# Performance work log

Measured on AMD Instinct MI355X. Metric: run time of the kernel, lower is better.

Reference implementation:

```python
import jax, jax.numpy as jnp
import numpy as np

N = 128          # cube side (voxels)
LPIX = 3.0       # Mpc per voxel (hardcoded in dsq_loss.forward)
KBINS = 100      # radial k bins (hardcoded)
LOSS_WEIGHT = 1.0


def _binning(n, lpix, kbins):
    # Static radial k-bin assignment computed once with numpy.
    kf = 2.0 * np.pi * np.fft.fftfreq(n, d=lpix)
    kx, ky, kz = np.meshgrid(kf, kf, kf, indexing='ij')
    kmag = np.sqrt(kx * kx + ky * ky + kz * kz).ravel()  # [n^3]
    pos = kmag > 0
    edges = np.linspace(kmag[pos].min(), kmag.max(), kbins + 1)
    ids = np.clip(np.digitize(kmag, edges) - 1, 0, kbins - 1)
    ids = np.where(pos, ids, kbins)  # route k=0 (DC) mode to a dropped bin
    counts = np.bincount(ids[pos], minlength=kbins).astype(np.float32)
    kcent = 0.5 * (edges[:-1] + edges[1:])
    return ids.astype(np.int32), counts, kcent.astype(np.float32)

_IDS, _COUNTS, _KCENT = _binning(N, LPIX, KBINS)


def _dsq(x):
    # x: [B, 1, N, N, N] -> dimensionless power spectrum Delta^2(k): [B, KBINS]
    b = x.shape[0]
    fk = jnp.fft.fftn(x, axes=(-3, -2, -1))
    # P(k) estimator: |delta_k|^2 * Lpix^3 / N^3  (Lpix^6/V with V=(N*Lpix)^3)
    pk = (fk.real ** 2 + fk.imag ** 2) * (LPIX ** 3 / float(N ** 3))
    pk = pk.reshape(b, -1).T  # [N^3, B]
    sums = jax.ops.segment_sum(pk, jnp.asarray(_IDS), num_segments=KBINS + 1)[:KBINS]
    cnt = jnp.asarray(_COUNTS)[:, None]
    pmean = jnp.where(cnt > 0, sums / jnp.maximum(cnt, 1.0), jnp.nan)  # [KBINS, B]
    kc = jnp.asarray(_KCENT)[:, None]
    dsq = pmean * kc ** 3 / (2.0 * jnp.pi ** 2)
    return dsq.T  # [B, KBINS]


def setup_inputs() -> dict:
    key = jax.random.key(0)
    k1, k2 = jax.random.split(key)
    # positive brightness-temperature-like fields so log10(Delta^2) is finite
    pred = jax.random.uniform(k1, (8, 1, N, N, N), dtype=jnp.float32) + 0.1
    target = jax.random.uniform(k2, (8, 1, N, N, N), dtype=jnp.float32) + 0.1
    return {"pred": pred, "target": target}


def reference(pred, target):
    dsq_hr = _dsq(target)
    dsq_sr = _dsq(pred)
    loss = jnp.nanmean(jnp.abs(jnp.log10(dsq_hr) - jnp.log10(dsq_sr)))
    return LOSS_WEIGHT * loss
```

## Files before the change

### kernel.cpp

```cpp
#include <hip/hip_runtime.h>
#include <math.h>

#ifndef M_PI
#define M_PI 3.14159265358979323846
#endif

#define NSIDE 128
#define NVOX  2097152
#define KBINS 100
#define NFIELDS 16
#define NORMF (27.0f / 2097152.0f)
#define FSTRIDE ((size_t)65 * 16384)

#define WS_SUMS_OFF   0
#define WS_CNT_OFF    6464
#define WS_OCT_OFF    8192
#define WS_TRANS_OFF  282880

__device__ __forceinline__ double bin_edge(int i, double start, double step, double stop) {
    if (i == 100) return stop;
    return __dadd_rn(__dmul_rn((double)i, step), start);
}

__device__ __forceinline__ void bin_params(double* start, double* step, double* stop) {
    const double inv   = 1.0 / 384.0;
    const double twopi = 2.0 * M_PI;
    double k1 = __dmul_rn(twopi, __dmul_rn(1.0, inv));
    *start = sqrt(__dadd_rn(__dadd_rn(0.0, 0.0), __dmul_rn(k1, k1)));
    double k64 = __dmul_rn(twopi, __dmul_rn(-64.0, inv));
    double s64 = __dmul_rn(k64, k64);
    *stop = sqrt(__dadd_rn(__dadd_rn(s64, s64), s64));
    *step = (*stop - *start) / 100.0;
}

__device__ int compute_bin(int ix, int iy, int iz) {
    const double inv   = 1.0 / 384.0;
    const double twopi = 2.0 * M_PI;
    double fx = (double)(ix < 64 ? ix : ix - 128);
    double fy = (double)(iy < 64 ? iy : iy - 128);
    double fz = (double)(iz < 64 ? iz : iz - 128);
    double kx = __dmul_rn(twopi, __dmul_rn(fx, inv));
    double ky = __dmul_rn(twopi, __dmul_rn(fy, inv));
    double kz = __dmul_rn(twopi, __dmul_rn(fz, inv));
    double sq = __dadd_rn(__dadd_rn(__dmul_rn(kx, kx), __dmul_rn(ky, ky)), __dmul_rn(kz, kz));
    double kmag = sqrt(sq);
    if (!(kmag > 0.0)) return 100;
    double start, step, stop;
    bin_params(&start, &step, &stop);
    double t = (kmag - start) / step;
    int c = (int)floor(t);
    if (c < -1) c = -1;
    if (c > 100) c = 100;
    while (c < 100 && kmag >= bin_edge(c + 1, start, step, stop)) ++c;
    while (c >= 0 && kmag < bin_edge(c, start, step, stop)) --c;
    if (c < 0) c = 0;
    if (c > 99) c = 99;
    return c;
}


__device__ __forceinline__ int br3(int v) { return ((v & 1) << 2) | (v & 2) | ((v >> 2) & 1); }
__device__ __forceinline__ int br4(int v) {
    return ((v & 1) << 3) | ((v & 2) << 1) | ((v & 4) >> 1) | ((v & 8) >> 3);
}

__device__ __forceinline__ float2 f2add(float2 a, float2 b) { return make_float2(a.x + b.x, a.y + b.y); }
__device__ __forceinline__ float2 f2sub(float2 a, float2 b) { return make_float2(a.x - b.x, a.y - b.y); }
__device__ __forceinline__ float2 cmul(float2 a, float2 w) {
    return make_float2(a.x * w.x - a.y * w.y, a.x * w.y + a.y * w.x);
}
__device__ __forceinline__ float2 twid(float r) {
    return make_float2(__builtin_amdgcn_cosf(r), __builtin_amdgcn_sinf(r));
}

__device__ __forceinline__ void fft128_r16(float2 r[16], int m) {
    const float fm = (float)m;
#pragma unroll
    for (int j = 0; j < 8; ++j) {
        float2 W = twid(-(fm + 8.0f * (float)j) * (1.0f / 128.0f));
        float2 a = r[j], b = r[j + 8];
        r[j]     = f2add(a, b);
        r[j + 8] = cmul(f2sub(a, b), W);
    }
#pragma unroll
    for (int j = 0; j < 4; ++j) {
        float2 W = twid(-(fm + 8.0f * (float)j) * (1.0f / 64.0f));
#pragma unroll
        for (int half = 0; half < 16; half += 8) {
            float2 a = r[half + j], b = r[half + j + 4];
            r[half + j]     = f2add(a, b);
            r[half + j + 4] = cmul(f2sub(a, b), W);
        }
    }
#pragma unroll
    for (int j = 0; j < 2; ++j) {
        float2 W = twid(-(fm + 8.0f * (float)j) * (1.0f / 32.0f));
#pragma unroll
        for (int q = 0; q < 16; q += 4) {
            float2 a = r[q + j], b = r[q + j + 2];
            r[q + j]     = f2add(a, b);
            r[q + j + 2] = cmul(f2sub(a, b), W);
        }
    }
    {
        float2 W = twid(-fm * (1.0f / 16.0f));
#pragma unroll
        for (int q = 0; q < 16; q += 2) {
            float2 a = r[q], b = r[q + 1];
            r[q]     = f2add(a, b);
            r[q + 1] = cmul(f2sub(a, b), W);
        }
    }
#pragma unroll
    for (int h = 4; h >= 2; h >>= 1) {
        bool hi = (m & h) != 0;
        float2 W = twid(-(float)(m & (h - 1)) / (float)(2 * h));
#pragma unroll
        for (int j = 0; j < 16; ++j) {
            float2 x = r[j];
            float2 v = make_float2(__shfl_xor(x.x, h, 64), __shfl_xor(x.y, h, 64));
            float2 s = f2add(x, v);
            float2 d = cmul(f2sub(v, x), W);
            r[j] = hi ? d : s;
        }
    }
    {
        bool hi = (m & 1) != 0;
#pragma unroll
        for (int j = 0; j < 16; ++j) {
            float2 x = r[j];
            float2 v = make_float2(__shfl_xor(x.x, 1, 64), __shfl_xor(x.y, 1, 64));
            r[j] = hi ? f2sub(v, x) : f2add(x, v);
        }
    }
}

__global__ __launch_bounds__(256) void k_zero(float* sums, int* counts) {
    int t = blockIdx.x * 256 + threadIdx.x;
    if (t < NFIELDS * 101) sums[t] = 0.0f;
    if (t < 101) counts[t] = 0;
}

__global__ __launch_bounds__(256) void k_oct(unsigned char* __restrict__ oct,
                                             int* __restrict__ counts) {
    __shared__ int lcnt[4][104];
    int tid = threadIdx.x;
#pragma unroll
    for (int j = tid; j < 4 * 104; j += 256) ((int*)lcnt)[j] = 0;
    __syncthreads();
    int idx = blockIdx.x * 256 + tid;
    if (idx < 65 * 65 * 65) {
        int c = idx % 65;
        int r = idx / 65;
        int b = r % 65;
        int a = r / 65;
        int id = compute_bin(a, b, c);
        oct[c * 4225 + a * 65 + b] = (unsigned char)id;
        if (id < 100) {
            int w = ((a == 0 || a == 64) ? 1 : 2) *
                    ((b == 0 || b == 64) ? 1 : 2) *
                    ((c == 0 || c == 64) ? 1 : 2);
            atomicAdd(&lcnt[tid & 3][id], w);
        }
    }
    __syncthreads();
    if (tid < 101) {
        int tot = lcnt[0][tid] + lcnt[1][tid] + lcnt[2][tid] + lcnt[3][tid];
        if (tot) atomicAdd(&counts[tid], tot);
    }
}

__global__ __launch_bounds__(256, 2) void k_fft_zy(const float* __restrict__ pred,
                                                   const float* __restrict__ target,
                                                   float2* __restrict__ A) {
    __shared__ float2 lds[65][130];
    int t = threadIdx.x;
    int m = t & 7, row = t >> 3;
    int x = blockIdx.x;
    int f = blockIdx.y;
    const float* in = (f < 8) ? (pred + (size_t)f * NVOX)
                              : (target + (size_t)(f - 8) * NVOX);

    int b3 = br3(m);
#pragma unroll
    for (int y0 = 0; y0 < 128; y0 += 32) {
        int y = y0 + row;
        const float* src = in + (size_t)x * 16384 + (size_t)y * 128;
        float2 r[16];
#pragma unroll
        for (int j = 0; j < 16; ++j) r[j] = make_float2(src[m + 8 * j], 0.0f);
        fft128_r16(r, m);
        if (b3 < 4) {
#pragma unroll
            for (int j = 0; j < 16; ++j) lds[16 * b3 + br4(j)][y] = r[j];
        } else if (b3 == 4) {
            lds[64][y] = r[0];
        }
    }
    __syncthreads();

    float2* basef = A + (size_t)f * FSTRIDE + (size_t)x * 128;
#pragma unroll
    for (int k0 = 0; k0 < 96; k0 += 32) {
        int kz = k0 + row;
        if (kz <= 64) {
            float2 r[16];
#pragma unroll
            for (int j = 0; j < 16; ++j) r[j] = lds[kz][m + 8 * j];
            fft128_r16(r, m);
            float2* dst = basef + (size_t)kz * 16384;
#pragma unroll
            for (int j = 0; j < 16; ++j) dst[m + 8 * j] = r[j];
        }
    }
}

__global__ __launch_bounds__(256, 6) void k_fft_x_bin(const float2* __restrict__ A,
                                                      const unsigned char* __restrict__ oct,
                                                      float* __restrict__ sums) {
    __shared__ float lbins[8][104];
    __shared__ unsigned char ltab[4225];
    int t = threadIdx.x;
    int m = t & 7, g = t >> 3;
    int kz = blockIdx.x >> 2;
    int s0 = (blockIdx.x & 3) << 5;
    int f = blockIdx.y;
    for (int j = t; j < 8 * 104; j += 256) ((float*)lbins)[j] = 0.0f;
    for (int j = t; j < 4225; j += 256) ltab[j] = oct[kz * 4225 + j];
    const float2* base = A + (size_t)f * FSTRIDE + (size_t)kz * 16384 + (s0 + g);
    float2 r[16];
#pragma unroll
    for (int j = 0; j < 16; ++j) r[j] = base[(size_t)(m + 8 * j) * 128];
    fft128_r16(r, m);
    __syncthreads();
    int p = s0 + g;
    int ky = (br3(p & 7) << 4) | br4(p >> 3);
    int mky = (ky <= 64) ? ky : 128 - ky;
    int b3x = br3(m) << 4;
#pragma unroll
    for (int j = 0; j < 16; ++j) {
        int kx = b3x | br4(j);
        int mkx = (kx <= 64) ? kx : 128 - kx;
        float pk = r[j].x * r[j].x + r[j].y * r[j].y;
        atomicAdd(&lbins[t & 7][ltab[mkx * 65 + mky]], pk);
    }
    __syncthreads();
    if (t < 101) {
        float wz = (kz == 0 || kz == 64) ? 1.0f : 2.0f;
        float v = lbins[0][t] + lbins[1][t] + lbins[2][t] + lbins[3][t] +
                  lbins[4][t] + lbins[5][t] + lbins[6][t] + lbins[7][t];
        if (v != 0.0f) atomicAdd(&sums[f * 101 + t], v * (NORMF) * wz);
    }
}

__global__ __launch_bounds__(128) void k_finalize(const float* __restrict__ sums,
                                                  const int* __restrict__ counts,
                                                  float* __restrict__ out) {
    __shared__ double ssum[128];
    __shared__ int scnt[128];
    int k = threadIdx.x;
    double local = 0.0;
    int nloc = 0;
    if (k < KBINS) {
        int c = counts[k];
        if (c > 0) {
            double start, step, stop;
            bin_params(&start, &step, &stop);
            double e0 = bin_edge(k, start, step, stop);
            double e1 = bin_edge(k + 1, start, step, stop);
            float kc  = (float)(0.5 * (e0 + e1));
            float kc3 = kc * kc * kc;
            const float two_pi2 = (float)(2.0 * M_PI * M_PI);
            float cf = (float)c;
            for (int b = 0; b < 8; ++b) {
                float pm_p = sums[b * 101 + k] / cf;
                float pm_t = sums[(8 + b) * 101 + k] / cf;
                float dsq_p = pm_p * kc3 / two_pi2;
                float dsq_t = pm_t * kc3 / two_pi2;
                float d = fabsf(log10f(dsq_t) - log10f(dsq_p));
                local += (double)d;
            }
            nloc = 8;
        }
    }
    ssum[k] = local;
    scnt[k] = nloc;
    __syncthreads();
    for (int off = 64; off > 0; off >>= 1) {
        if (k < off) { ssum[k] += ssum[k + off]; scnt[k] += scnt[k + off]; }
        __syncthreads();
    }
    if (k == 0) out[0] = (float)(ssum[0] / (double)scnt[0]);
}

extern "C" void kernel_launch(void* const* d_in, const int* in_sizes, int n_in,
                              void* d_out, int out_size, void* d_ws, size_t ws_size,
                              hipStream_t stream) {
    (void)in_sizes; (void)n_in; (void)out_size; (void)ws_size;
    const float* pred   = (const float*)d_in[0];
    const float* target = (const float*)d_in[1];
    float* out = (float*)d_out;
    char* ws = (char*)d_ws;

    float* sums        = (float*)(ws + WS_SUMS_OFF);
    int* counts        = (int*)(ws + WS_CNT_OFF);
    unsigned char* oct = (unsigned char*)(ws + WS_OCT_OFF);
    float2* A          = (float2*)(ws + WS_TRANS_OFF);

    k_zero<<<7, 256, 0, stream>>>(sums, counts);
    k_oct<<<(65 * 65 * 65 + 255) / 256, 256, 0, stream>>>(oct, counts);

    k_fft_zy<<<dim3(128, NFIELDS), 256, 0, stream>>>(pred, target, A);
    k_fft_x_bin<<<dim3(65 * 4, NFIELDS), 256, 0, stream>>>(A, oct, sums);

    k_finalize<<<1, 128, 0, stream>>>(sums, counts, out);
}
```

Before: 333.6 us.

## Vectorize z-FFT input loads with new contiguous FFT and retile intermediate layout

Replaces the strided per-element z-row loads with float4 loads of 16 contiguous samples per lane, paired with a new FFT variant (fft128_c16) that uses precomputed constant twiddles suited to that contiguous assignment. It changes the intermediate spectrum layout so both the y-pass stores and the x-pass loads touch more contiguous addresses, and pads the LDS row to 132. It also adds scheduling barriers after the loads. The new FFT and layout must stay consistent with the bit-reversal indexing used later, which adds correctness risk.

```diff
diff --git a/kernel.cpp b/kernel.cpp
--- a/kernel.cpp
+++ b/kernel.cpp
@@ -11,6 +11,7 @@
 #define NFIELDS 16
 #define NORMF (27.0f / 2097152.0f)
 #define FSTRIDE ((size_t)65 * 16384)
+
 
 #define WS_SUMS_OFF   0
 #define WS_CNT_OFF    6464
@@ -58,7 +59,6 @@
     return c;
 }
 
-
 __device__ __forceinline__ int br3(int v) { return ((v & 1) << 2) | (v & 2) | ((v >> 2) & 1); }
 __device__ __forceinline__ int br4(int v) {
     return ((v & 1) << 3) | ((v & 2) << 1) | ((v & 4) >> 1) | ((v & 8) >> 3);
@@ -131,6 +131,107 @@
             float2 x = r[j];
             float2 v = make_float2(__shfl_xor(x.x, 1, 64), __shfl_xor(x.y, 1, 64));
             r[j] = hi ? f2sub(v, x) : f2add(x, v);
+        }
+    }
+}
+
+__device__ __forceinline__ void fft128_c16(float2 r[16], int m) {
+    const float S2 = 0.70710678118654752f;
+    {
+        int q = m & 3;
+        float2 Wm = make_float2(q == 0 ? 1.f : (q == 1 ? S2 : (q == 2 ? 0.f : -S2)),
+                                q == 0 ? 0.f : (q == 2 ? -1.f : -S2));
+        bool hi = (m & 4) != 0;
+        const float2 C[16] = {
+            {1.f,0.f},{0.99879546f,-0.04906767f},{0.99518473f,-0.09801714f},
+            {0.98917651f,-0.14673047f},{0.98078528f,-0.19509032f},{0.97003125f,-0.24298018f},
+            {0.95694034f,-0.29028468f},{0.94154407f,-0.33688985f},{0.92387953f,-0.38268343f},
+            {0.90398929f,-0.42755509f},{0.88192126f,-0.47139674f},{0.85772861f,-0.51410274f},
+            {0.83146961f,-0.55557023f},{0.80320753f,-0.59569930f},{0.77301045f,-0.63439328f},
+            {0.74095113f,-0.67155895f} };
+#pragma unroll
+        for (int j = 0; j < 16; ++j) {
+            float2 x = r[j];
+            float2 v = make_float2(__shfl_xor(x.x, 4, 64), __shfl_xor(x.y, 4, 64));
+            float2 s = f2add(x, v);
+            float2 d = cmul(cmul(f2sub(v, x), Wm), C[j]);
+            r[j] = hi ? d : s;
+        }
+    }
+    {
+        bool w = (m & 1) != 0;
+        bool hi = (m & 2) != 0;
+        const float2 C[16] = {
+            {1.f,0.f},{0.99518473f,-0.09801714f},{0.98078528f,-0.19509032f},
+            {0.95694034f,-0.29028468f},{0.92387953f,-0.38268343f},{0.88192126f,-0.47139674f},
+            {0.83146961f,-0.55557023f},{0.77301045f,-0.63439328f},{S2,-S2},
+            {0.63439328f,-0.77301045f},{0.55557023f,-0.83146961f},{0.47139674f,-0.88192126f},
+            {0.38268343f,-0.92387953f},{0.29028468f,-0.95694034f},{0.19509032f,-0.98078528f},
+            {0.09801714f,-0.99518473f} };
+#pragma unroll
+        for (int j = 0; j < 16; ++j) {
+            float2 x = r[j];
+            float2 v = make_float2(__shfl_xor(x.x, 2, 64), __shfl_xor(x.y, 2, 64));
+            float2 s = f2add(x, v);
+            float2 d = f2sub(v, x);
+            d = w ? make_float2(d.y, -d.x) : d;
+            d = cmul(d, C[j]);
+            r[j] = hi ? d : s;
+        }
+    }
+    {
+        bool hi = (m & 1) != 0;
+        const float2 C[16] = {
+            {1.f,0.f},{0.98078528f,-0.19509032f},{0.92387953f,-0.38268343f},
+            {0.83146961f,-0.55557023f},{S2,-S2},{0.55557023f,-0.83146961f},
+            {0.38268343f,-0.92387953f},{0.19509032f,-0.98078528f},{0.f,-1.f},
+            {-0.19509032f,-0.98078528f},{-0.38268343f,-0.92387953f},{-0.55557023f,-0.83146961f},
+            {-S2,-S2},{-0.83146961f,-0.55557023f},{-0.92387953f,-0.38268343f},
+            {-0.98078528f,-0.19509032f} };
+#pragma unroll
+        for (int j = 0; j < 16; ++j) {
+            float2 x = r[j];
+            float2 v = make_float2(__shfl_xor(x.x, 1, 64), __shfl_xor(x.y, 1, 64));
+            float2 s = f2add(x, v);
+            float2 d = cmul(f2sub(v, x), C[j]);
+            r[j] = hi ? d : s;
+        }
+    }
+    {
+        const float2 C[8] = {
+            {1.f,0.f},{0.92387953f,-0.38268343f},{S2,-S2},{0.38268343f,-0.92387953f},
+            {0.f,-1.f},{-0.38268343f,-0.92387953f},{-S2,-S2},{-0.92387953f,-0.38268343f} };
+#pragma unroll
+        for (int j = 0; j < 8; ++j) {
+            float2 a = r[j], b = r[j + 8];
+            r[j]     = f2add(a, b);
+            r[j + 8] = cmul(f2sub(a, b), C[j]);
+        }
+    }
+    {
+        const float2 C[4] = { {1.f,0.f},{S2,-S2},{0.f,-1.f},{-S2,-S2} };
+#pragma unroll
+        for (int q = 0; q < 16; q += 8)
+#pragma unroll
+            for (int j = 0; j < 4; ++j) {
+                float2 a = r[q + j], b = r[q + j + 4];
+                r[q + j]     = f2add(a, b);
+                r[q + j + 4] = cmul(f2sub(a, b), C[j]);
+            }
+    }
+    {
+#pragma unroll
+        for (int q = 0; q < 16; q += 4) {
+            { float2 a = r[q], b = r[q + 2]; r[q] = f2add(a, b); r[q + 2] = f2sub(a, b); }
+            { float2 a = r[q + 1], b = r[q + 3]; float2 d = f2sub(a, b);
+              r[q + 1] = f2add(a, b); r[q + 3] = make_float2(d.y, -d.x); }
+        }
+    }
+    {
+#pragma unroll
+        for (int q = 0; q < 16; q += 2) {
+            float2 a = r[q], b = r[q + 1];
+            r[q] = f2add(a, b); r[q + 1] = f2sub(a, b);
         }
     }
 }
@@ -173,7 +274,7 @@
 __global__ __launch_bounds__(256, 2) void k_fft_zy(const float* __restrict__ pred,
                                                    const float* __restrict__ target,
                                                    float2* __restrict__ A) {
-    __shared__ float2 lds[65][130];
+    __shared__ float2 lds[65][132];
     int t = threadIdx.x;
     int m = t & 7, row = t >> 3;
     int x = blockIdx.x;
@@ -185,21 +286,29 @@
 #pragma unroll
     for (int y0 = 0; y0 < 128; y0 += 32) {
         int y = y0 + row;
-        const float* src = in + (size_t)x * 16384 + (size_t)y * 128;
+        const float4* s4 = reinterpret_cast<const float4*>(
+            in + (size_t)x * 16384 + (size_t)y * 128 + 16 * m);
         float2 r[16];
 #pragma unroll
-        for (int j = 0; j < 16; ++j) r[j] = make_float2(src[m + 8 * j], 0.0f);
-        fft128_r16(r, m);
-        if (b3 < 4) {
-#pragma unroll
-            for (int j = 0; j < 16; ++j) lds[16 * b3 + br4(j)][y] = r[j];
-        } else if (b3 == 4) {
-            lds[64][y] = r[0];
-        }
-    }
-    __syncthreads();
-
-    float2* basef = A + (size_t)f * FSTRIDE + (size_t)x * 128;
+        for (int q = 0; q < 4; ++q) {
+            float4 v = s4[q];
+            r[4 * q + 0] = make_float2(v.x, 0.f);
+            r[4 * q + 1] = make_float2(v.y, 0.f);
+            r[4 * q + 2] = make_float2(v.z, 0.f);
+            r[4 * q + 3] = make_float2(v.w, 0.f);
+        }
+        __builtin_amdgcn_sched_barrier(0);
+        fft128_c16(r, m);
+#pragma unroll
+        for (int j = 0; j < 16; j += 2) {
+            int kz = 8 * br4(j) + b3;
+            lds[kz][y] = r[j];
+        }
+        if (m == 0) lds[64][y] = r[1];
+    }
+    __syncthreads();
+
+    float2* basef = A + (size_t)f * FSTRIDE + (size_t)x * 8;
 #pragma unroll
     for (int k0 = 0; k0 < 96; k0 += 32) {
         int kz = k0 + row;
@@ -207,10 +316,11 @@
             float2 r[16];
 #pragma unroll
             for (int j = 0; j < 16; ++j) r[j] = lds[kz][m + 8 * j];
+            __builtin_amdgcn_sched_barrier(0);
             fft128_r16(r, m);
             float2* dst = basef + (size_t)kz * 16384;
 #pragma unroll
-            for (int j = 0; j < 16; ++j) dst[m + 8 * j] = r[j];
+            for (int j = 0; j < 16; ++j) dst[j * 1024 + m] = r[j];
         }
     }
 }
@@ -227,13 +337,15 @@
     int f = blockIdx.y;
     for (int j = t; j < 8 * 104; j += 256) ((float*)lbins)[j] = 0.0f;
     for (int j = t; j < 4225; j += 256) ltab[j] = oct[kz * 4225 + j];
-    const float2* base = A + (size_t)f * FSTRIDE + (size_t)kz * 16384 + (s0 + g);
+    int p = s0 + g;
+    const float2* base = A + (size_t)f * FSTRIDE + (size_t)kz * 16384
+                           + (size_t)(p >> 3) * 1024 + (p & 7);
     float2 r[16];
 #pragma unroll
-    for (int j = 0; j < 16; ++j) r[j] = base[(size_t)(m + 8 * j) * 128];
+    for (int j = 0; j < 16; ++j) r[j] = base[8 * m + 64 * j];
+    __builtin_amdgcn_sched_barrier(0);
     fft128_r16(r, m);
     __syncthreads();
-    int p = s0 + g;
     int ky = (br3(p & 7) << 4) | br4(p >> 3);
     int mky = (ky <= 64) ? ky : 128 - ky;
     int b3x = br3(m) << 4;
```

Result: no change. 334.3 us (+0.2%).
